# Optimization experiments

Hardware: AMD Instinct MI355X
Metric: run time of the kernel (lower is better)

The kernel has to match this reference:

```python
import jax, jax.numpy as jnp
import numpy as np

IN_F, OUT_F, GROUP, BITS = 4096, 11008, 128, 4
PACK = 32 // BITS            # 8 nibbles per int32 word
N_GROUPS = IN_F // GROUP     # 32
MASK = (1 << BITS) - 1       # 0xF
TOKENS = 2048


def setup_inputs() -> dict:
    key = jax.random.key(0)
    ks = jax.random.split(key, 6)
    x = jax.random.normal(ks[0], (TOKENS, IN_F), dtype=jnp.float32)
    qweight = jax.random.randint(ks[1], (IN_F // PACK, OUT_F), 0, 2147483647, dtype=jnp.int32)
    qzeros = jax.random.randint(ks[2], (N_GROUPS, OUT_F // PACK), 0, 2147483647, dtype=jnp.int32)
    qscales = jax.random.randint(ks[3], (N_GROUPS, OUT_F), 0, 256, dtype=jnp.int32)  # uint8 values
    qscales_zeros = jax.random.uniform(ks[4], (1, OUT_F), dtype=jnp.float32)
    qscales_scales = jax.random.uniform(ks[5], (1, OUT_F), dtype=jnp.float32) * 0.01
    g_idx = jnp.arange(IN_F, dtype=jnp.int32) // GROUP
    return dict(x=x, qweight=qweight, qzeros=qzeros, qscales=qscales,
                qscales_zeros=qscales_zeros, qscales_scales=qscales_scales, g_idx=g_idx)


def _dequantize(qweight, qzeros, qscales, qscales_zeros, qscales_scales, g_idx, dtype):
    shifts = jnp.arange(0, 32, BITS, dtype=jnp.int32)  # [8]
    # unpack weights: [in/8, 8, out] -> [in, out]
    w = (qweight[:, None, :] >> shifts[None, :, None]) & MASK
    w = w.reshape(-1, qweight.shape[-1])
    # unpack zero-points (+1 per original code): [n_groups, out/8, 8] -> [n_groups, out]
    z = (((qzeros[:, :, None] >> shifts[None, None, :]) & MASK) + 1)
    z = z.reshape(-1, qweight.shape[-1])
    # dequantize the uint8-quantized scales, then apply group-wise
    scales = (qscales.astype(dtype) - qscales_zeros) * qscales_scales  # [n_groups, out]
    return (w - z[g_idx]).astype(dtype) * scales[g_idx]                # [in, out]


def reference(x, qweight, qzeros, qscales, qscales_zeros, qscales_scales, g_idx):
    weight = _dequantize(qweight, qzeros, qscales, qscales_zeros, qscales_scales,
                         g_idx, x.dtype)
    return x @ weight  # bias disabled (disable_bias=True)
```

## Files before the change

kernel.cpp:

```cpp
#include <hip/hip_runtime.h>
#include <hip/hip_fp16.h>
#include <stdint.h>

#define IN_F   4096
#define OUT_F  11008
#define TOKENS 2048
#define BM 128
#define BN 64
#define BK 64
#define NT (IN_F / BK)
#define NGROUP 32
#define OPW (OUT_F / 8)

typedef _Float16 f16;
typedef __attribute__((ext_vector_type(2))) _Float16 f16x2;
typedef __attribute__((ext_vector_type(8))) _Float16 f16x8;
typedef __attribute__((ext_vector_type(4))) float f32x4;
typedef __attribute__((ext_vector_type(4))) int   i32x4;

typedef __attribute__((address_space(3))) uint32_t lds_u32_t;
typedef const __attribute__((address_space(1))) uint32_t glb_u32_t;

#define SB0() __builtin_amdgcn_sched_barrier(0)

static __device__ __forceinline__ void gload_lds16(const void* g, void* l) {
    __builtin_amdgcn_global_load_lds((glb_u32_t*)g, (lds_u32_t*)l, 16, 0, 0);
}

__global__ __launch_bounds__(256) void quant_x_kernel(const float* __restrict__ x,
                                                      char* __restrict__ xi,
                                                      float* __restrict__ aws) {
    __shared__ float red[4];
    const int row = blockIdx.x;
    const int tid = threadIdx.x;
    const float* xr = x + (size_t)row * IN_F + tid * 16;
    float v[16];
    #pragma unroll
    for (int p = 0; p < 4; ++p) {
        const float4 t = *reinterpret_cast<const float4*>(xr + p * 4);
        v[p * 4 + 0] = t.x; v[p * 4 + 1] = t.y; v[p * 4 + 2] = t.z; v[p * 4 + 3] = t.w;
    }
    float m = 0.f;
    #pragma unroll
    for (int p = 0; p < 16; ++p) m = fmaxf(m, fabsf(v[p]));
    #pragma unroll
    for (int off = 32; off > 0; off >>= 1) m = fmaxf(m, __shfl_xor(m, off));
    if ((tid & 63) == 0) red[tid >> 6] = m;
    __syncthreads();
    m = fmaxf(fmaxf(red[0], red[1]), fmaxf(red[2], red[3]));
    const float a   = m * (1.0f / 127.0f);
    const float inv = (m > 0.f) ? 127.0f / m : 0.f;
    if (tid == 0) aws[row] = a;
    const float MAGIC = 12582912.0f;
    uint32_t b[16];
    #pragma unroll
    for (int p = 0; p < 16; ++p)
        b[p] = __builtin_bit_cast(uint32_t, fmaf(v[p], inv, MAGIC)) & 0xFFu;
    i32x4 d;
    d[0] = (int)(b[0] | (b[2] << 8) | (b[4]  << 16) | (b[6]  << 24));
    d[1] = (int)(b[1] | (b[3] << 8) | (b[5]  << 16) | (b[7]  << 24));
    d[2] = (int)(b[8] | (b[10] << 8) | (b[12] << 16) | (b[14] << 24));
    d[3] = (int)(b[9] | (b[11] << 8) | (b[13] << 16) | (b[15] << 24));
    *reinterpret_cast<i32x4*>(xi + (size_t)row * IN_F + tid * 16) = d;
}

__global__ __launch_bounds__(256, 4) void qgemm_i8_kernel(
    const char*     __restrict__ xi,
    const float*    __restrict__ aws,
    const uint32_t* __restrict__ qweight,
    const uint32_t* __restrict__ qzeros,
    const int*      __restrict__ qscales,
    const float*    __restrict__ qscales_zeros,
    const float*    __restrict__ qscales_scales,
    float*          __restrict__ out)
{
    __shared__ __align__(16) char Ash[2][BM * BK];
    __shared__ __align__(16) char Bsh[2][BN * BK];

    const int tid  = threadIdx.x;
    const int lane = tid & 63;
    const int wid  = tid >> 6;
    const int wm   = wid >> 1;
    const int wn   = wid & 1;

    const int mt = blockIdx.x & 15;
    const int nt = blockIdx.x >> 4;
    const int m0 = mt * BM;
    const int n0 = nt * BN;

    const int colb = tid & 63;
    const int h    = tid >> 6;
    const int ncol = n0 + colb;
    const int boff = colb * BK + (h ^ ((colb >> 1) & 3)) * 16;
    const uint32_t* bptr = qweight + (size_t)(2 * h) * OUT_F + ncol;

    const int arow = tid >> 2;
    const int aunit = (tid & 3) ^ ((arow >> 1) & 3);
    const char* asrc0 = xi + (size_t)(m0 + arow) * IN_F + aunit * 16;
    const int adst0 = tid * 16, adst1 = (tid + 256) * 16;

    const int lr = lane & 15;
    const int lo = lane >> 4;
    int aoffr[4], boffr[2];
    #pragma unroll
    for (int f = 0; f < 4; ++f) {
        const int ra = wm * 64 + f * 16 + lr;
        aoffr[f] = ra * BK + ((lo ^ ((ra >> 1) & 3))) * 16;
    }
    #pragma unroll
    for (int j = 0; j < 2; ++j) {
        const int rb = wn * 32 + j * 16 + lr;
        boffr[j] = rb * BK + ((lo ^ ((rb >> 1) & 3))) * 16;
    }
    const int cread0 = n0 + wn * 32 + lr;
    const int cread1 = cread0 + 16;
    float qszr[2], qssr[2];
    qszr[0] = qscales_zeros[cread0]; qssr[0] = qscales_scales[cread0];
    qszr[1] = qscales_zeros[cread1]; qssr[1] = qscales_scales[cread1];

    f32x4 acc[4][2];
    #pragma unroll
    for (int i = 0; i < 4; ++i)
        #pragma unroll
        for (int j = 0; j < 2; ++j) {
            f32x4 z = {0.f, 0.f, 0.f, 0.f};
            acc[i][j] = z;
        }
    i32x4 D[4][2];

    auto load_bw = [&](int t_, uint32_t* w) {
        const uint32_t* p = bptr + (size_t)t_ * 8 * OUT_F;
        w[0] = p[0];
        w[1] = p[OUT_F];
    };
    auto mk_kz = [&](uint32_t zw_) -> uint32_t {
        const uint32_t znib = (zw_ >> ((ncol & 7) * 4)) & 0xFu;
        return (127u - znib) * 0x01010101u;
    };
    auto stage_B = [&](int buf, const uint32_t* w, uint32_t kz) {
        i32x4 d;
        d[0] = (int)((((w[0]      ) & 0x0F0F0F0Fu) + kz) ^ 0x80808080u);
        d[1] = (int)((((w[0] >> 4 ) & 0x0F0F0F0Fu) + kz) ^ 0x80808080u);
        d[2] = (int)((((w[1]      ) & 0x0F0F0F0Fu) + kz) ^ 0x80808080u);
        d[3] = (int)((((w[1] >> 4 ) & 0x0F0F0F0Fu) + kz) ^ 0x80808080u);
        *reinterpret_cast<i32x4*>(&Bsh[buf][boff]) = d;
    };
    auto stage_A = [&](int buf, int t_) {
        gload_lds16(asrc0 + (size_t)t_ * BK, &Ash[buf][adst0]);
        gload_lds16(asrc0 + (size_t)t_ * BK + (size_t)64 * IN_F, &Ash[buf][adst1]);
    };
    auto flushD = [&](const int* sf) {
        float scur[2];
        #pragma unroll
        for (int j = 0; j < 2; ++j)
            scur[j] = ((float)sf[j] - qszr[j]) * qssr[j];
        #pragma unroll
        for (int i = 0; i < 4; ++i)
            #pragma unroll
            for (int j = 0; j < 2; ++j) {
                acc[i][j].x += scur[j] * (float)D[i][j][0];
                acc[i][j].y += scur[j] * (float)D[i][j][1];
                acc[i][j].z += scur[j] * (float)D[i][j][2];
                acc[i][j].w += scur[j] * (float)D[i][j][3];
            }
    };

    uint32_t wE[2], wO[2];
    uint32_t zwE, zwO;
    int sfE[2], sfO[2];

    {
        uint32_t w00[2];
        load_bw(0, w00);
        const uint32_t zw0 = qzeros[ncol >> 3];
        stage_A(0, 0);
        stage_B(0, w00, mk_kz(zw0));
        load_bw(1, wE);
        zwE = qzeros[ncol >> 3];
        sfE[0] = qscales[cread0];
        sfE[1] = qscales[cread1];
        asm volatile("s_waitcnt vmcnt(0)" ::: "memory");
        asm volatile("s_waitcnt lgkmcnt(0)" ::: "memory");
        __builtin_amdgcn_s_barrier();
    }

#define BODY(C, T, WC, ZC, WL, ZL, SFL, CHAIN, DOFLUSH, SFLUSH)                   \
  {                                                                               \
    const int tn1_ = ((T) + 1 < NT) ? (T) + 1 : NT - 1;                           \
    const int tn2_ = ((T) + 2 < NT) ? (T) + 2 : NT - 1;                           \
    const int gz_  = ((T) + 2) >> 1 < NGROUP ? ((T) + 2) >> 1 : NGROUP - 1;       \
    const int gs_  = ((T) + 1) >> 1 < NGROUP ? ((T) + 1) >> 1 : NGROUP - 1;       \
    stage_B((C) ^ 1, WC, mk_kz(ZC));                                              \
    stage_A((C) ^ 1, tn1_);                                                       \
    if (DOFLUSH) { flushD(SFLUSH); }      \
    SB0();                                                                        \
    load_bw(tn2_, WL);                                                            \
    ZL = qzeros[(size_t)gz_ * OPW + (ncol >> 3)];                                 \
    SFL[0] = qscales[(size_t)gs_ * OUT_F + cread0];                               \
    SFL[1] = qscales[(size_t)gs_ * OUT_F + cread1];                               \
    SB0();                                                                        \
    {                                                                             \
      i32x4 af[4], bf[2];                                                         \
      _Pragma("unroll") for (int f = 0; f < 4; ++f)                               \
        af[f] = *reinterpret_cast<const i32x4*>(&Ash[C][aoffr[f]]);               \
      _Pragma("unroll") for (int j = 0; j < 2; ++j)                               \
        bf[j] = *reinterpret_cast<const i32x4*>(&Bsh[C][boffr[j]]);               \
      __builtin_amdgcn_s_setprio(1);                                              \
      if (CHAIN) {                                                                \
        _Pragma("unroll") for (int i = 0; i < 4; ++i)                             \
          _Pragma("unroll") for (int j = 0; j < 2; ++j)                           \
            D[i][j] = __builtin_amdgcn_mfma_i32_16x16x64_i8(af[i], bf[j],         \
                                                            D[i][j], 0, 0, 0);   \
      } else {                                                                    \
        _Pragma("unroll") for (int i = 0; i < 4; ++i)                             \
          _Pragma("unroll") for (int j = 0; j < 2; ++j) {                         \
            i32x4 z0_ = {0, 0, 0, 0};                                             \
            D[i][j] = __builtin_amdgcn_mfma_i32_16x16x64_i8(af[i], bf[j],         \
                                                            z0_, 0, 0, 0);       \
          }                                                                       \
      }                                                                           \
      __builtin_amdgcn_s_setprio(0);                                              \
    }                                                                             \
    asm volatile("s_waitcnt vmcnt(5)" ::: "memory");                              \
    asm volatile("s_waitcnt lgkmcnt(0)" ::: "memory");                            \
    __builtin_amdgcn_s_barrier();                                                 \
  }

    BODY(0, 0, wE, zwE, wO, zwO, sfO, false, false, sfO)
    BODY(1, 1, wO, zwO, wE, zwE, sfE, true,  false, sfE)
    for (int t = 2; t < NT; t += 2) {
        BODY(0, t,     wE, zwE, wO, zwO, sfO, false, true,  sfO)
        BODY(1, t + 1, wO, zwO, wE, zwE, sfE, true,  false, sfE)
    }
#undef BODY
    flushD(sfO);

    const int orow = m0 + wm * 64 + lo * 4;
    const int ocol = n0 + wn * 32 + lr;
    #pragma unroll
    for (int i = 0; i < 4; ++i)
        #pragma unroll
        for (int j = 0; j < 2; ++j)
            #pragma unroll
            for (int r = 0; r < 4; ++r) {
                const int rr = orow + i * 16 + r;
                out[(size_t)rr * OUT_F + ocol + j * 16] = aws[rr] * acc[i][j][r];
            }
}

static __device__ __forceinline__ f16x8 dequant8(uint32_t w, f16x2 sv, f16x2 zv) {
    uint32_t p0 = (w & 0x000F000Fu) | 0x64006400u;
    uint32_t p1 = ((w >> 4)  & 0x000F000Fu) | 0x64006400u;
    uint32_t p2 = ((w >> 8)  & 0x000F000Fu) | 0x64006400u;
    uint32_t p3 = ((w >> 12) & 0x000F000Fu) | 0x64006400u;
    f16x2 h0 = (__builtin_bit_cast(f16x2, p0) + zv) * sv;
    f16x2 h1 = (__builtin_bit_cast(f16x2, p1) + zv) * sv;
    f16x2 h2 = (__builtin_bit_cast(f16x2, p2) + zv) * sv;
    f16x2 h3 = (__builtin_bit_cast(f16x2, p3) + zv) * sv;
    f16x8 o;
    o[0] = h0[0]; o[1] = h0[1]; o[2] = h1[0]; o[3] = h1[1];
    o[4] = h2[0]; o[5] = h2[1]; o[6] = h3[0]; o[7] = h3[1];
    return o;
}

__global__ __launch_bounds__(512, 4) void qgemm_f16_fb(
    const float* __restrict__ x, const uint32_t* __restrict__ qweight,
    const uint32_t* __restrict__ qzeros, const int* __restrict__ qscales,
    const float* __restrict__ qscales_zeros, const float* __restrict__ qscales_scales,
    float* __restrict__ out)
{
    __shared__ __align__(16) f16 heap[2][256 * 64];
    f16* const Ab0 = &heap[0][0];
    f16* const Ab1 = &heap[1][0];
    f16* const Bb0 = &heap[0][128 * 64];
    f16* const Bb1 = &heap[1][128 * 64];
    const int tid = threadIdx.x, lane = tid & 63, wid = tid >> 6;
    const int kg = wid >> 2, wm = (wid >> 1) & 1, wn = wid & 1;
    const int mt = blockIdx.x & 15, nt = blockIdx.x >> 4;
    const int m0 = mt * 128, n0 = nt * 128;
    const int colb = tid & 127, og2 = (tid >> 7) << 1, ncol = n0 + colb;
    const float ssv = qscales_scales[ncol], qzssv = qscales_zeros[ncol] * ssv;
    int bo[2];
    #pragma unroll
    for (int r = 0; r < 2; ++r) bo[r] = colb * 64 + ((og2 + r) ^ (colb & 7)) * 8;
    const uint32_t* bptr = qweight + (size_t)og2 * OUT_F + ncol;
    const int arow = tid >> 3, aoct = (tid & 7) ^ (arow & 7);
    const float* fsrc0 = x + (size_t)(m0 + arow) * IN_F + aoct * 8;
    const int aoff0 = tid * 8, aoff1 = (tid + 512) * 8;
    const int lr = lane & 15, lo = lane >> 4, koct = kg * 4 + lo;
    int offA[4], offB[4];
    #pragma unroll
    for (int f = 0; f < 4; ++f) {
        const int ra = wm * 64 + f * 16 + lr;
        offA[f] = ra * 64 + (koct ^ (ra & 7)) * 8;
        const int rb = wn * 64 + f * 16 + lr;
        offB[f] = rb * 64 + (koct ^ (rb & 7)) * 8;
    }
    f32x4 acc[4][4];
    #pragma unroll
    for (int i = 0; i < 4; ++i)
        #pragma unroll
        for (int j = 0; j < 4; ++j) { f32x4 z = {0,0,0,0}; acc[i][j] = z; }
    auto load_bw = [&](int t_, uint32_t* w) {
        const uint32_t* p = bptr + (size_t)t_ * 8 * OUT_F;
        w[0] = p[0]; w[1] = p[OUT_F];
    };
    auto mkc = [&](f16x2& sv_, f16x2& zv_, int sw_, uint32_t zw_) {
        const float sf = (float)sw_ * ssv - qzssv;
        const int z = (int)((zw_ >> ((ncol & 7) * 4)) & 0xFu);
        const f16 sh = (f16)sf, zh = (f16)(float)(-(1025 + z));
        sv_[0] = sh; sv_[1] = sh; zv_[0] = zh; zv_[1] = zh;
    };
    auto stage_B = [&](f16* Bb, const uint32_t* w, f16x2 sv_, f16x2 zv_) {
        *reinterpret_cast<f16x8*>(&Bb[bo[0]]) = dequant8(w[0], sv_, zv_);
        *reinterpret_cast<f16x8*>(&Bb[bo[1]]) = dequant8(w[1], sv_, zv_);
    };
    auto stage_A = [&](f16* Ab, int t_) {
        #pragma unroll
        for (int i = 0; i < 2; ++i) {
            const float* p = fsrc0 + (size_t)t_ * 64 + (size_t)(64 * i) * IN_F;
            const float4 v0 = *reinterpret_cast<const float4*>(p);
            const float4 v1 = *reinterpret_cast<const float4*>(p + 4);
            f16x8 v;
            v[0] = (f16)v0.x; v[1] = (f16)v1.x; v[2] = (f16)v0.y; v[3] = (f16)v1.y;
            v[4] = (f16)v0.z; v[5] = (f16)v1.z; v[6] = (f16)v0.w; v[7] = (f16)v1.w;
            *reinterpret_cast<f16x8*>(&Ab[i == 0 ? aoff0 : aoff1]) = v;
        }
    };
    auto compute = [&](const f16* Ab, const f16* Bb) {
        f16x8 af[4], bf[4];
        #pragma unroll
        for (int f = 0; f < 4; ++f) af[f] = *reinterpret_cast<const f16x8*>(&Ab[offA[f]]);
        #pragma unroll
        for (int f = 0; f < 4; ++f) bf[f] = *reinterpret_cast<const f16x8*>(&Bb[offB[f]]);
        #pragma unroll
        for (int i = 0; i < 4; ++i)
            #pragma unroll
            for (int j = 0; j < 4; ++j)
                acc[i][j] = __builtin_amdgcn_mfma_f32_16x16x32_f16(af[i], bf[j], acc[i][j], 0, 0, 0);
    };
    uint32_t wcur[2], wnxt[2];
    int swN; uint32_t zwN;
    f16x2 sv, zv, svN, zvN;
    {
        uint32_t w0[2];
        load_bw(0, w0);
        const int sw0 = qscales[ncol];
        const uint32_t zw0 = qzeros[ncol >> 3];
        stage_A(Ab0, 0);
        load_bw(1, wcur);
        swN = qscales[OUT_F + ncol]; zwN = qzeros[OPW + (ncol >> 3)];
        mkc(sv, zv, sw0, zw0);
        stage_B(Bb0, w0, sv, zv);
        asm volatile("s_waitcnt lgkmcnt(0)" ::: "memory");
        __builtin_amdgcn_s_barrier();
    }
    for (int t = 0; t < 64; t += 2) {
        mkc(svN, zvN, swN, zwN);
        stage_B(Bb1, wcur, sv, zv);
        stage_A(Ab1, t + 1);
        load_bw(t + 2 < 64 ? t + 2 : 63, wnxt);
        {
            const int g2 = (t >> 1) + 2 < NGROUP ? (t >> 1) + 2 : NGROUP - 1;
            swN = qscales[(size_t)g2 * OUT_F + ncol];
            zwN = qzeros[(size_t)g2 * OPW + (ncol >> 3)];
        }
        compute(Ab0, Bb0);
        asm volatile("s_waitcnt lgkmcnt(0)" ::: "memory");
        __builtin_amdgcn_s_barrier();
        sv = svN; zv = zvN;
        stage_B(Bb0, wnxt, sv, zv);
        stage_A(Ab0, t + 2 < 64 ? t + 2 : 63);
        load_bw(t + 3 < 64 ? t + 3 : 63, wcur);
        compute(Ab1, Bb1);
        asm volatile("s_waitcnt lgkmcnt(0)" ::: "memory");
        __builtin_amdgcn_s_barrier();
    }
    __syncthreads();
    f32x4* scratch = reinterpret_cast<f32x4*>(&heap[0][0]);
    const int wpos = wid & 3;
    #pragma unroll
    for (int hh = 0; hh < 2; ++hh) {
        if (kg == 1) {
            #pragma unroll
            for (int di = 0; di < 2; ++di)
                #pragma unroll
                for (int j = 0; j < 4; ++j)
                    scratch[wpos * 512 + (di * 4 + j) * 64 + lane] = acc[2 * hh + di][j];
        }
        __syncthreads();
        if (kg == 0) {
            #pragma unroll
            for (int di = 0; di < 2; ++di)
                #pragma unroll
                for (int j = 0; j < 4; ++j) {
                    const f32x4 p = scratch[wpos * 512 + (di * 4 + j) * 64 + lane];
                    acc[2 * hh + di][j].x += p.x; acc[2 * hh + di][j].y += p.y;
                    acc[2 * hh + di][j].z += p.z; acc[2 * hh + di][j].w += p.w;
                }
        }
        __syncthreads();
    }
    if (kg == 0) {
        const int orow = m0 + wm * 64 + lo * 4;
        const int ocol = n0 + wn * 64 + lr;
        #pragma unroll
        for (int i = 0; i < 4; ++i)
            #pragma unroll
            for (int j = 0; j < 4; ++j)
                #pragma unroll
                for (int r = 0; r < 4; ++r)
                    out[(size_t)(orow + i * 16 + r) * OUT_F + ocol + j * 16] = acc[i][j][r];
    }
}

extern "C" void kernel_launch(void* const* d_in, const int* in_sizes, int n_in,
                              void* d_out, int out_size, void* d_ws, size_t ws_size,
                              hipStream_t stream) {
    const float*    xp  = (const float*)d_in[0];
    const uint32_t* qw  = (const uint32_t*)d_in[1];
    const uint32_t* qz  = (const uint32_t*)d_in[2];
    const int*      qs  = (const int*)d_in[3];
    const float*    qsz = (const float*)d_in[4];
    const float*    qss = (const float*)d_in[5];
    float* outp = (float*)d_out;

    const size_t need = (size_t)TOKENS * IN_F + (size_t)TOKENS * 4;

    if (ws_size >= need) {
        char*  xi  = (char*)d_ws;
        float* aws = (float*)(xi + (size_t)TOKENS * IN_F);
        quant_x_kernel<<<TOKENS, 256, 0, stream>>>(xp, xi, aws);
        const int grid = (TOKENS / BM) * (OUT_F / BN);
        qgemm_i8_kernel<<<grid, 256, 0, stream>>>(xi, aws, qw, qz, qs, qsz, qss, outp);
    } else {
        const int gridf = (TOKENS / 128) * (OUT_F / 128);
        qgemm_f16_fb<<<gridf, 512, 0, stream>>>(xp, qw, qz, qs, qsz, qss, outp);
    }
}
```

Before: 176.5 us.

## Pre-swizzle quantized activations into MFMA fragment order and load A directly to registers

```diff
diff --git a/kernel.cpp b/kernel.cpp
--- a/kernel.cpp
+++ b/kernel.cpp
@@ -23,10 +23,6 @@
 
 #define SB0() __builtin_amdgcn_sched_barrier(0)
 
-static __device__ __forceinline__ void gload_lds16(const void* g, void* l) {
-    __builtin_amdgcn_global_load_lds((glb_u32_t*)g, (lds_u32_t*)l, 16, 0, 0);
-}
-
 __global__ __launch_bounds__(256) void quant_x_kernel(const float* __restrict__ x,
                                                       char* __restrict__ xi,
                                                       float* __restrict__ aws) {
@@ -61,7 +57,8 @@
     d[1] = (int)(b[1] | (b[3] << 8) | (b[5]  << 16) | (b[7]  << 24));
     d[2] = (int)(b[8] | (b[10] << 8) | (b[12] << 16) | (b[14] << 24));
     d[3] = (int)(b[9] | (b[11] << 8) | (b[13] << 16) | (b[15] << 24));
-    *reinterpret_cast<i32x4*>(xi + (size_t)row * IN_F + tid * 16) = d;
+    const size_t cidx = (size_t)(row >> 4) * 4096 + (size_t)tid * 16 + (row & 15);
+    *reinterpret_cast<i32x4*>(xi + cidx * 16) = d;
 }
 
 __global__ __launch_bounds__(256, 4) void qgemm_i8_kernel(
@@ -74,7 +71,6 @@
     const float*    __restrict__ qscales_scales,
     float*          __restrict__ out)
 {
-    __shared__ __align__(16) char Ash[2][BM * BK];
     __shared__ __align__(16) char Bsh[2][BN * BK];
 
     const int tid  = threadIdx.x;
@@ -94,19 +90,16 @@
     const int boff = colb * BK + (h ^ ((colb >> 1) & 3)) * 16;
     const uint32_t* bptr = qweight + (size_t)(2 * h) * OUT_F + ncol;
 
-    const int arow = tid >> 2;
-    const int aunit = (tid & 3) ^ ((arow >> 1) & 3);
-    const char* asrc0 = xi + (size_t)(m0 + arow) * IN_F + aunit * 16;
-    const int adst0 = tid * 16, adst1 = (tid + 256) * 16;
-
     const int lr = lane & 15;
     const int lo = lane >> 4;
-    int aoffr[4], boffr[2];
+    const char* a2base[4];
     #pragma unroll
     for (int f = 0; f < 4; ++f) {
-        const int ra = wm * 64 + f * 16 + lr;
-        aoffr[f] = ra * BK + ((lo ^ ((ra >> 1) & 3))) * 16;
-    }
+        const int g = mt * 8 + wm * 4 + f;
+        a2base[f] = xi + ((size_t)g * 4096 + lane) * 16;
+    }
+
+    int boffr[2];
     #pragma unroll
     for (int j = 0; j < 2; ++j) {
         const int rb = wn * 32 + j * 16 + lr;
@@ -145,9 +138,10 @@
         d[3] = (int)((((w[1] >> 4 ) & 0x0F0F0F0Fu) + kz) ^ 0x80808080u);
         *reinterpret_cast<i32x4*>(&Bsh[buf][boff]) = d;
     };
-    auto stage_A = [&](int buf, int t_) {
-        gload_lds16(asrc0 + (size_t)t_ * BK, &Ash[buf][adst0]);
-        gload_lds16(asrc0 + (size_t)t_ * BK + (size_t)64 * IN_F, &Ash[buf][adst1]);
+    auto load_af = [&](i32x4* dst, int t_) {
+        #pragma unroll
+        for (int f = 0; f < 4; ++f)
+            dst[f] = *reinterpret_cast<const i32x4*>(a2base[f] + (size_t)t_ * 1024);
     };
     auto flushD = [&](const int* sf) {
         float scur[2];
@@ -168,12 +162,13 @@
     uint32_t wE[2], wO[2];
     uint32_t zwE, zwO;
     int sfE[2], sfO[2];
+    i32x4 afA[4], afB[4];
 
     {
         uint32_t w00[2];
         load_bw(0, w00);
         const uint32_t zw0 = qzeros[ncol >> 3];
-        stage_A(0, 0);
+        load_af(afA, 0);
         stage_B(0, w00, mk_kz(zw0));
         load_bw(1, wE);
         zwE = qzeros[ncol >> 3];
@@ -184,14 +179,14 @@
         __builtin_amdgcn_s_barrier();
     }
 
-#define BODY(C, T, WC, ZC, WL, ZL, SFL, CHAIN, DOFLUSH, SFLUSH)                   \
+#define BODY(C, T, WC, ZC, WL, ZL, SFL, CHAIN, DOFLUSH, SFLUSH, AFC, AFN)         \
   {                                                                               \
     const int tn1_ = ((T) + 1 < NT) ? (T) + 1 : NT - 1;                           \
     const int tn2_ = ((T) + 2 < NT) ? (T) + 2 : NT - 1;                           \
     const int gz_  = ((T) + 2) >> 1 < NGROUP ? ((T) + 2) >> 1 : NGROUP - 1;       \
     const int gs_  = ((T) + 1) >> 1 < NGROUP ? ((T) + 1) >> 1 : NGROUP - 1;       \
     stage_B((C) ^ 1, WC, mk_kz(ZC));                                              \
-    stage_A((C) ^ 1, tn1_);                                                       \
+    load_af(AFN, tn1_);                                                           \
     if (DOFLUSH) { flushD(SFLUSH); }      \
     SB0();                                                                        \
     load_bw(tn2_, WL);                                                            \
@@ -200,37 +195,34 @@
     SFL[1] = qscales[(size_t)gs_ * OUT_F + cread1];                               \
     SB0();                                                                        \
     {                                                                             \
-      i32x4 af[4], bf[2];                                                         \
-      _Pragma("unroll") for (int f = 0; f < 4; ++f)                               \
-        af[f] = *reinterpret_cast<const i32x4*>(&Ash[C][aoffr[f]]);               \
+      i32x4 bf[2];                                                                \
       _Pragma("unroll") for (int j = 0; j < 2; ++j)                               \
         bf[j] = *reinterpret_cast<const i32x4*>(&Bsh[C][boffr[j]]);               \
       __builtin_amdgcn_s_setprio(1);                                              \
       if (CHAIN) {                                                                \
         _Pragma("unroll") for (int i = 0; i < 4; ++i)                             \
           _Pragma("unroll") for (int j = 0; j < 2; ++j)                           \
-            D[i][j] = __builtin_amdgcn_mfma_i32_16x16x64_i8(af[i], bf[j],         \
+            D[i][j] = __builtin_amdgcn_mfma_i32_16x16x64_i8(AFC[i], bf[j],        \
                                                             D[i][j], 0, 0, 0);   \
       } else {                                                                    \
         _Pragma("unroll") for (int i = 0; i < 4; ++i)                             \
           _Pragma("unroll") for (int j = 0; j < 2; ++j) {                         \
             i32x4 z0_ = {0, 0, 0, 0};                                             \
-            D[i][j] = __builtin_amdgcn_mfma_i32_16x16x64_i8(af[i], bf[j],         \
+            D[i][j] = __builtin_amdgcn_mfma_i32_16x16x64_i8(AFC[i], bf[j],        \
                                                             z0_, 0, 0, 0);       \
           }                                                                       \
       }                                                                           \
       __builtin_amdgcn_s_setprio(0);                                              \
     }                                                                             \
-    asm volatile("s_waitcnt vmcnt(5)" ::: "memory");                              \
     asm volatile("s_waitcnt lgkmcnt(0)" ::: "memory");                            \
     __builtin_amdgcn_s_barrier();                                                 \
   }
 
-    BODY(0, 0, wE, zwE, wO, zwO, sfO, false, false, sfO)
-    BODY(1, 1, wO, zwO, wE, zwE, sfE, true,  false, sfE)
+    BODY(0, 0, wE, zwE, wO, zwO, sfO, false, false, sfO, afA, afB)
+    BODY(1, 1, wO, zwO, wE, zwE, sfE, true,  false, sfE, afB, afA)
     for (int t = 2; t < NT; t += 2) {
-        BODY(0, t,     wE, zwE, wO, zwO, sfO, false, true,  sfO)
-        BODY(1, t + 1, wO, zwO, wE, zwE, sfE, true,  false, sfE)
+        BODY(0, t,     wE, zwE, wO, zwO, sfO, false, true,  sfO, afA, afB)
+        BODY(1, t + 1, wO, zwO, wE, zwE, sfE, true,  false, sfE, afB, afA)
     }
 #undef BODY
     flushD(sfO);
```

Measured after the change: 509.1 us. 188% more time.
